# Kernel tuning notes

Measured on AMD Instinct MI355X. Metric: run time of the kernel, lower is better.

The kernel has to match this reference:

```python
import jax, jax.numpy as jnp
import numpy as np

N, E, D, L = 40000, 640000, 128, 4

def setup_inputs() -> dict:
    key = jax.random.key(0)
    ks = jax.random.split(key, 4)
    x = jax.random.normal(ks[0], (N, D), dtype=jnp.float32)
    edge_index = jax.random.randint(ks[1], (2, E), 0, N)
    edge_weight = jax.random.uniform(ks[2], (E,), dtype=jnp.float32)
    W = jax.random.normal(ks[3], (L, D, D), dtype=jnp.float32) / np.float32(np.sqrt(D))
    b = jnp.zeros((L, D), jnp.float32)
    gamma = jnp.ones((L, D), jnp.float32)
    beta = jnp.zeros((L, D), jnp.float32)
    return dict(x=x, edge_index=edge_index, edge_weight=edge_weight, W=W, b=b, gamma=gamma, beta=beta)

def _gcn_norm(edge_index, edge_weight, n):
    # PyG gcn_norm: add self loops (weight 1), symmetric D^-1/2 A D^-1/2
    loops = jnp.arange(n)
    src = jnp.concatenate([edge_index[0], loops])
    dst = jnp.concatenate([edge_index[1], loops])
    ew = jnp.concatenate([edge_weight, jnp.ones((n,), edge_weight.dtype)])
    deg = jax.ops.segment_sum(ew, dst, num_segments=n)
    dis = jnp.where(deg > 0, jax.lax.rsqrt(jnp.maximum(deg, 1e-12)), 0.0)
    return src, dst, dis[src] * ew * dis[dst]

def _batchnorm(h, g, bta):
    # training-mode BatchNorm1d over the node axis, biased variance, eps=1e-5
    mu = h.mean(0)
    var = h.var(0)
    return g * (h - mu) * jax.lax.rsqrt(var + 1e-5) + bta

def reference(x, edge_index, edge_weight, W, b, gamma, beta):
    n = x.shape[0]
    n_layers = W.shape[0]
    src, dst, norm = _gcn_norm(edge_index, edge_weight, n)
    x0 = x  # decoded_reshaped_x for skip connections
    for i in range(n_layers):
        h = x @ W[i]                                   # [N, D] linear (GCNConv.lin)
        msg = h[src] * norm[:, None]                   # gather + scale, [E+N, D]
        h = jax.ops.segment_sum(msg, dst, num_segments=n) + b[i]
        if i < n_layers - 1:
            h = jax.nn.relu(h)
        h = h + x0                                     # skip connection
        if i != n_layers - 2:
            h = _batchnorm(h, gamma[i], beta[i])
        x = h
    return x
```

## Files before the change

### kernel.cpp

```cpp
#include <hip/hip_runtime.h>
#include <cstdint>
#include <cstddef>

constexpr int N = 40000;
constexpr int E = 640000;
constexpr int D = 128;
constexpr int NBLK = (N + 255) / 256;
constexpr int NBKT = NBLK;
constexpr int BCAP = 5120;
constexpr int AGG_GRID = 2500;

typedef _Float16 half8 __attribute__((ext_vector_type(8)));
typedef float f32x4 __attribute__((ext_vector_type(4)));

__device__ __forceinline__ unsigned int pack_rec(int idx, float v) {
  union { _Float16 h; unsigned short us; } c; c.h = (_Float16)v;
  return (unsigned int)idx | ((unsigned int)c.us << 16);
}


__global__ void k_zero(uint4* __restrict__ p, uint4* __restrict__ q) {
  int i = blockIdx.x * 256 + threadIdx.x;
  if (i < 22096) p[i] = make_uint4(0u, 0u, 0u, 0u);
  else if (i < 22136) q[i - 22096] = make_uint4(0u, 0u, 0u, 0u);
}


__global__ void k_bigprep(const int* __restrict__ ei, const float* __restrict__ ew,
                          unsigned long long* __restrict__ packed,
                          const float* __restrict__ X, _Float16* __restrict__ Xh,
                          const float* __restrict__ W, _Float16* __restrict__ Wt,
                          unsigned long long* __restrict__ binned,
                          int* __restrict__ bktcnt) {
  int bid = blockIdx.x, t = threadIdx.x;
  if (bid < 313) {
    __shared__ int lhist[NBKT], lbase[NBKT], lrank[NBKT];
    if (t < NBKT) { lhist[t] = 0; lrank[t] = 0; }
    __syncthreads();
    int e8 = bid * 256 + t;
    bool act = (e8 < E / 8);
    int4 sa, sb, da, db; float4 wa, wb;
    if (act) {
      sa = ((const int4*)ei)[e8 * 2];
      sb = ((const int4*)ei)[e8 * 2 + 1];
      da = ((const int4*)(ei + E))[e8 * 2];
      db = ((const int4*)(ei + E))[e8 * 2 + 1];
      wa = ((const float4*)ew)[e8 * 2];
      wb = ((const float4*)ew)[e8 * 2 + 1];
      atomicAdd(&packed[da.x], (1ULL << 40) | (unsigned long long)__float2uint_rn(wa.x * 67108864.0f));
      atomicAdd(&packed[da.y], (1ULL << 40) | (unsigned long long)__float2uint_rn(wa.y * 67108864.0f));
      atomicAdd(&packed[da.z], (1ULL << 40) | (unsigned long long)__float2uint_rn(wa.z * 67108864.0f));
      atomicAdd(&packed[da.w], (1ULL << 40) | (unsigned long long)__float2uint_rn(wa.w * 67108864.0f));
      atomicAdd(&packed[db.x], (1ULL << 40) | (unsigned long long)__float2uint_rn(wb.x * 67108864.0f));
      atomicAdd(&packed[db.y], (1ULL << 40) | (unsigned long long)__float2uint_rn(wb.y * 67108864.0f));
      atomicAdd(&packed[db.z], (1ULL << 40) | (unsigned long long)__float2uint_rn(wb.z * 67108864.0f));
      atomicAdd(&packed[db.w], (1ULL << 40) | (unsigned long long)__float2uint_rn(wb.w * 67108864.0f));
      atomicAdd(&lhist[da.x >> 8], 1); atomicAdd(&lhist[da.y >> 8], 1);
      atomicAdd(&lhist[da.z >> 8], 1); atomicAdd(&lhist[da.w >> 8], 1);
      atomicAdd(&lhist[db.x >> 8], 1); atomicAdd(&lhist[db.y >> 8], 1);
      atomicAdd(&lhist[db.z >> 8], 1); atomicAdd(&lhist[db.w >> 8], 1);
    }
    __syncthreads();
    if (t < NBKT && lhist[t] > 0) lbase[t] = atomicAdd(&bktcnt[t], lhist[t]);
    __syncthreads();
    if (act) {
      auto emit = [&](int s, int dcol, float w) {
        int bkt = dcol >> 8;
        int rank = atomicAdd(&lrank[bkt], 1);
        int pos = lbase[bkt] + rank;
        unsigned long long rec = (unsigned long long)pack_rec(s, w)
                               | ((unsigned long long)(dcol & 255) << 32);
        if (pos < BCAP) binned[(size_t)bkt * BCAP + pos] = rec;
      };
      emit(sa.x, da.x, wa.x); emit(sa.y, da.y, wa.y);
      emit(sa.z, da.z, wa.z); emit(sa.w, da.w, wa.w);
      emit(sb.x, db.x, wb.x); emit(sb.y, db.y, wb.y);
      emit(sb.z, db.z, wb.z); emit(sb.w, db.w, wb.w);
    }
  } else if (bid < 2813) {
    int i = (bid - 313) * 256 + t;
    float4 v0 = ((const float4*)X)[i * 2];
    float4 v1 = ((const float4*)X)[i * 2 + 1];
    half8 h;
    h[0] = (_Float16)v0.x; h[1] = (_Float16)v0.y; h[2] = (_Float16)v0.z; h[3] = (_Float16)v0.w;
    h[4] = (_Float16)v1.x; h[5] = (_Float16)v1.y; h[6] = (_Float16)v1.z; h[7] = (_Float16)v1.w;
    ((half8*)Xh)[i] = h;
  } else {
    int o = (bid - 2813) * 256 + t;
    int l = o >> 14, rem = o & 16383, c = rem >> 7, k = rem & 127;
    Wt[o] = (_Float16)W[l * 16384 + k * 128 + c];
  }
}

__global__ __launch_bounds__(256) void k_partial(const unsigned long long* __restrict__ packed,
                                                 int* __restrict__ bsum) {
  __shared__ int red[256];
  int t = threadIdx.x;
  int i = blockIdx.x * 256 + t;
  red[t] = (i < N) ? ((int)(packed[i] >> 40) + 1) : 0;
  __syncthreads();
  for (int off = 128; off > 0; off >>= 1) {
    if (t < off) red[t] += red[t + off];
    __syncthreads();
  }
  if (t == 0) bsum[blockIdx.x] = red[0];
}

__global__ void k_scan_bsums(const int* __restrict__ bsum, int* __restrict__ bpre) {
  __shared__ int s[256];
  int t = threadIdx.x;
  s[t] = (t < NBLK) ? bsum[t] : 0;
  __syncthreads();
  for (int off = 1; off < 256; off <<= 1) {
    int v = s[t];
    int add = (t >= off) ? s[t - off] : 0;
    __syncthreads();
    s[t] = v + add;
    __syncthreads();
  }
  if (t < NBLK) bpre[t] = (t == 0) ? 0 : s[t - 1];
}

__global__ __launch_bounds__(256) void k_fill_offs(const unsigned long long* __restrict__ packed,
    const int* __restrict__ bpre, int* __restrict__ offs,
    unsigned int* __restrict__ cv, float* __restrict__ dis, int* __restrict__ hist) {
  __shared__ int s[256];
  __shared__ int lhist[64];
  int t = threadIdx.x;
  int i = blockIdx.x * 256 + t;
  if (t < 64) lhist[t] = 0;
  unsigned long long p = (i < N) ? packed[i] : 0ULL;
  int c = (i < N) ? ((int)(p >> 40) + 1) : 0;
  s[t] = c;
  __syncthreads();
  for (int off = 1; off < 256; off <<= 1) {
    int v = s[t];
    int add = (t >= off) ? s[t - off] : 0;
    __syncthreads();
    s[t] = v + add;
    __syncthreads();
  }
  if (i < N) {
    float deg = (float)(p & ((1ULL << 40) - 1)) * (1.0f / 67108864.0f);
    float ds = rsqrtf(deg + 1.0f);
    dis[i] = ds;
    int run = bpre[blockIdx.x] + s[t] - c;
    offs[i] = run;
    cv[run] = pack_rec(i, 1.0f);
    atomicAdd(&lhist[min(c, 63)], 1);
  }
  __syncthreads();
  if (t < 64 && lhist[t] > 0) atomicAdd(&hist[t], lhist[t]);
  if (i == N - 1) offs[N] = N + E;
}


__global__ void k_histscan(const int* __restrict__ hist, int* __restrict__ histstart,
                           int* __restrict__ histcur) {
  int b = threadIdx.x;
  int s = 0;
  for (int b2 = b + 1; b2 < 64; ++b2) s += hist[b2];
  histstart[b] = s;
  histcur[b] = s;
}


__device__ __forceinline__ void gemm_body(int bid, int tid, const _Float16* __restrict__ X,
    const _Float16* __restrict__ Wt, const float* __restrict__ sums,
    const float* __restrict__ gamma, const float* __restrict__ beta, int useBN,
    const float* __restrict__ dis, _Float16* __restrict__ Hout,
    float* scl, float* shf) {
  if (tid < 128) {
    if (useBN) {
      float s = 0.f, s2 = 0.f;
#pragma unroll
      for (int r = 0; r < 8; ++r) { s += sums[r * 256 + tid]; s2 += sums[r * 256 + 128 + tid]; }
      float mu = s * (1.0f / N);
      float var = s2 * (1.0f / N) - mu * mu;
      float rs = rsqrtf(var + 1e-5f);
      float sc = gamma[tid] * rs;
      scl[tid] = sc;
      shf[tid] = beta[tid] - mu * sc;
    } else {
      scl[tid] = 1.0f;
      shf[tid] = 0.0f;
    }
  }
  __syncthreads();

  int wv = tid >> 6, lane = tid & 63;
  int fr = lane & 15, kg = lane >> 4;
  int arow = bid * 64 + wv * 16 + fr;
  const _Float16* xrow = X + (size_t)arow * D;

  half8 af[4];
#pragma unroll
  for (int kc = 0; kc < 4; ++kc) {
    int k0 = kc * 32 + kg * 8;
    half8 xr = *(const half8*)&xrow[k0];
    half8 a;
#pragma unroll
    for (int u = 0; u < 8; ++u)
      a[u] = (_Float16)fmaf((float)xr[u], scl[k0 + u], shf[k0 + u]);
    af[kc] = a;
  }

  f32x4 acc[8];
#pragma unroll
  for (int ct = 0; ct < 8; ++ct) acc[ct] = (f32x4){0.f, 0.f, 0.f, 0.f};

#pragma unroll
  for (int ct = 0; ct < 8; ++ct) {
    const _Float16* wcol = Wt + (size_t)(ct * 16 + fr) * 128;
#pragma unroll
    for (int kc = 0; kc < 4; ++kc) {
      half8 bf = *(const half8*)&wcol[kc * 32 + kg * 8];
      acc[ct] = __builtin_amdgcn_mfma_f32_16x16x32_f16(af[kc], bf, acc[ct], 0, 0, 0);
    }
  }

  int orow0 = bid * 64 + wv * 16 + kg * 4;
#pragma unroll
  for (int rg = 0; rg < 4; ++rg) {
    int grow = orow0 + rg;
    float dsv = dis[grow];
    _Float16* hrow = Hout + (size_t)grow * D;
#pragma unroll
    for (int ct = 0; ct < 8; ++ct)
      hrow[ct * 16 + fr] = (_Float16)(acc[ct][rg] * dsv);
  }
}

__global__ __launch_bounds__(256) void k_gemm(const _Float16* __restrict__ X,
    const _Float16* __restrict__ Wt, const float* __restrict__ sums,
    const float* __restrict__ gamma, const float* __restrict__ beta, int useBN,
    const float* __restrict__ dis, _Float16* __restrict__ Hout) {
  __shared__ float scl[128], shf[128];
  gemm_body(blockIdx.x, threadIdx.x, X, Wt, sums, gamma, beta, useBN, dis, Hout, scl, shf);
}


__global__ __launch_bounds__(256) void k_gemm0_fill(const _Float16* __restrict__ X,
    const _Float16* __restrict__ Wt, const float* __restrict__ dis,
    _Float16* __restrict__ Hout,
    const int* __restrict__ offs, const unsigned long long* __restrict__ binned,
    const int* __restrict__ bktcnt, unsigned int* __restrict__ cv,
    const unsigned long long* __restrict__ packed, int* __restrict__ histcur,
    int* __restrict__ perm) {
  int bid = blockIdx.x, t = threadIdx.x;
  if (bid < 625) {
    __shared__ float scl[128], shf[128];
    gemm_body(bid, t, X, Wt, (const float*)nullptr, (const float*)nullptr,
              (const float*)nullptr, 0, dis, Hout, scl, shf);
  } else if (bid < 625 + NBKT) {
    int bkt = bid - 625;
    __shared__ int lcur[256];
    int row = bkt * 256 + t;
    lcur[t] = (row < N) ? (offs[row] + 1) : 0;
    __syncthreads();
    int cnt = min(bktcnt[bkt], BCAP);
    const unsigned long long* bp = binned + (size_t)bkt * BCAP;
    for (int e = t; e < cnt; e += 256) {
      unsigned long long r = bp[e];
      int local = (int)(r >> 32);
      int slot = atomicAdd(&lcur[local], 1);
      cv[slot] = (unsigned int)r;
    }
  } else {
    __shared__ int lhist[64], lbase[64];
    if (t < 64) lhist[t] = 0;
    __syncthreads();
    int i = (bid - (625 + NBKT)) * 256 + t;
    bool valid = (i < N);
    int bin = 0, myrank = 0;
    if (valid) {
      int c = (int)(packed[i] >> 40) + 1;
      bin = min(c, 63);
      myrank = atomicAdd(&lhist[bin], 1);
    }
    __syncthreads();
    if (t < 64 && lhist[t] > 0) lbase[t] = atomicAdd(&histcur[t], lhist[t]);
    __syncthreads();
    if (valid) perm[lbase[bin] + myrank] = i;
  }
}


__global__ __launch_bounds__(256) void k_agg(const uint4* __restrict__ Hu4,
    const int* __restrict__ offs, const unsigned int* __restrict__ cv,
    const float* __restrict__ dis, const float* __restrict__ bias,
    const uint4* __restrict__ x0h, const int* __restrict__ perm,
    int doRelu, int doStats, int outF32,
    _Float16* __restrict__ Hout16, float* __restrict__ Houtf, float* __restrict__ sums) {
  int t = threadIdx.x;
  int sl = t & 15;
  int g = t >> 4;
  int row = perm[blockIdx.x * 16 + g];
  float4 bv0 = ((const float4*)bias)[sl * 2];
  float4 bv1 = ((const float4*)bias)[sl * 2 + 1];

  int e0 = offs[row], e1 = offs[row + 1];
  float a[8];
#pragma unroll
  for (int k = 0; k < 8; ++k) a[k] = 0.f;
  for (int eb = e0; eb < e1; eb += 16) {
    int m = min(16, e1 - eb);
    unsigned int rec = 0;
    if (sl < m) rec = cv[eb + sl];
#pragma unroll 8
    for (int j = 0; j < m; ++j) {
      unsigned int rj = __shfl(rec, j, 16);
      int sj = (int)(rj & 0xFFFFu);
      union { unsigned short us; _Float16 h; } vh; vh.us = (unsigned short)(rj >> 16);
      float vj = (float)vh.h;
      union { uint4 u; _Float16 hh[8]; } cu;
      cu.u = Hu4[(size_t)sj * 16 + sl];
#pragma unroll
      for (int k = 0; k < 8; ++k) a[k] = fmaf((float)cu.hh[k], vj, a[k]);
    }
  }
  float dr = dis[row];
  union { uint4 u; _Float16 hh[8]; } xc;
  xc.u = x0h[(size_t)row * 16 + sl];
  float rr[8];
  rr[0] = fmaf(a[0], dr, bv0.x); rr[1] = fmaf(a[1], dr, bv0.y);
  rr[2] = fmaf(a[2], dr, bv0.z); rr[3] = fmaf(a[3], dr, bv0.w);
  rr[4] = fmaf(a[4], dr, bv1.x); rr[5] = fmaf(a[5], dr, bv1.y);
  rr[6] = fmaf(a[6], dr, bv1.z); rr[7] = fmaf(a[7], dr, bv1.w);
  if (doRelu) {
#pragma unroll
    for (int k = 0; k < 8; ++k) rr[k] = fmaxf(rr[k], 0.f);
  }
#pragma unroll
  for (int k = 0; k < 8; ++k) rr[k] += (float)xc.hh[k];
  if (outF32) {
    float4 o0, o1;
    o0.x = rr[0]; o0.y = rr[1]; o0.z = rr[2]; o0.w = rr[3];
    o1.x = rr[4]; o1.y = rr[5]; o1.z = rr[6]; o1.w = rr[7];
    ((float4*)Houtf)[(size_t)row * 32 + sl * 2] = o0;
    ((float4*)Houtf)[(size_t)row * 32 + sl * 2 + 1] = o1;
  } else {
    union { uint4 u; _Float16 hh[8]; } ov;
#pragma unroll
    for (int k = 0; k < 8; ++k) ov.hh[k] = (_Float16)rr[k];
    ((uint4*)Hout16)[(size_t)row * 16 + sl] = ov.u;
  }

  if (doStats) {
    __shared__ float reds[16 * 128], reds2[16 * 128];
#pragma unroll
    for (int k = 0; k < 8; ++k) {
      reds[g * 128 + sl * 8 + k] = rr[k];
      reds2[g * 128 + sl * 8 + k] = rr[k] * rr[k];
    }
    __syncthreads();
    if (t < 128) {
      float ts = 0.f, ts2 = 0.f;
#pragma unroll
      for (int j = 0; j < 16; ++j) { ts += reds[j * 128 + t]; ts2 += reds2[j * 128 + t]; }
      int rep = blockIdx.x & 7;
      atomicAdd(&sums[rep * 256 + t], ts);
      atomicAdd(&sums[rep * 256 + 128 + t], ts2);
    }
  }
}


__global__ __launch_bounds__(256) void k_bnapply(float* __restrict__ H,
    const float* __restrict__ sums, const float* __restrict__ gamma,
    const float* __restrict__ beta) {
  __shared__ float scl[128], shf[128];
  int t = threadIdx.x;
  if (t < 128) {
    float s = 0.f, s2 = 0.f;
#pragma unroll
    for (int r = 0; r < 8; ++r) { s += sums[r * 256 + t]; s2 += sums[r * 256 + 128 + t]; }
    float mu = s * (1.0f / N);
    float var = s2 * (1.0f / N) - mu * mu;
    float rs = rsqrtf(var + 1e-5f);
    float sc = gamma[t] * rs;
    scl[t] = sc;
    shf[t] = beta[t] - mu * sc;
  }
  __syncthreads();
  size_t i = (size_t)blockIdx.x * 256 + t;
  float4 v = ((const float4*)H)[i];
  int c = (int)(i & 31) * 4;
  v.x = fmaf(v.x, scl[c + 0], shf[c + 0]);
  v.y = fmaf(v.y, scl[c + 1], shf[c + 1]);
  v.z = fmaf(v.z, scl[c + 2], shf[c + 2]);
  v.w = fmaf(v.w, scl[c + 3], shf[c + 3]);
  ((float4*)H)[i] = v;
}


extern "C" void kernel_launch(void* const* d_in, const int* in_sizes, int n_in,
                              void* d_out, int out_size, void* d_ws, size_t ws_size,
                              hipStream_t stream) {
  const float* x     = (const float*)d_in[0];
  const int*   ei    = (const int*)d_in[1];
  const float* ew    = (const float*)d_in[2];
  const float* W     = (const float*)d_in[3];
  const float* b     = (const float*)d_in[4];
  const float* gamma = (const float*)d_in[5];
  const float* beta  = (const float*)d_in[6];
  float* out = (float*)d_out;

  char* ws = (char*)d_ws;
  _Float16* hlin   = (_Float16*)ws;
  _Float16* hagg16 = (_Float16*)(ws + 10240000);
  _Float16* xh     = (_Float16*)(ws + 20480000);
  unsigned long long* packed = (unsigned long long*)(ws + 30720000);
  float* sums4    = (float*)(ws + 31040000);
  int*   hist     = (int*)  (ws + 31072768);
  int*   histstart= (int*)  (ws + 31073024);
  int*   histcur  = (int*)  (ws + 31073280);
  float* dis      = (float*)(ws + 31073536);
  int*   offs     = (int*)  (ws + 31233536);
  int*   bktcnt   = (int*)  (ws + 31393552);
  unsigned int* cv= (unsigned int*)(ws + 31553552);
  int*   perm     = (int*)  (ws + 34273552);
  int*   bsum     = (int*)  (ws + 34433552);
  int*   bpre     = (int*)  (ws + 34434192);
  _Float16* Wt    = (_Float16*)(ws + 34434832);
  unsigned long long* binned = (unsigned long long*)(ws + 34565904);

  k_zero<<<87, 256, 0, stream>>>((uint4*)packed, (uint4*)bktcnt);
  k_bigprep<<<3069, 256, 0, stream>>>(ei, ew, packed, x, xh, W, Wt, binned, bktcnt);
  k_partial<<<NBLK, 256, 0, stream>>>(packed, bsum);
  k_scan_bsums<<<1, 256, 0, stream>>>(bsum, bpre);
  k_fill_offs<<<NBLK, 256, 0, stream>>>(packed, bpre, offs, cv, dis, hist);
  k_histscan<<<1, 64, 0, stream>>>(hist, histstart, histcur);

  for (int l = 0; l < 4; ++l) {
    const _Float16* xin = (l == 0) ? xh : hagg16;
    if (l == 0) {
      k_gemm0_fill<<<625 + NBKT + 157, 256, 0, stream>>>(xin, Wt, dis, hlin,
                                                         offs, binned, bktcnt, cv,
                                                         packed, histcur, perm);
    } else {
      int useBN = (l == 1 || l == 2) ? 1 : 0;
      const float* sprev = sums4 + (size_t)(l - 1) * 2048;
      k_gemm<<<N / 64, 256, 0, stream>>>(xin, Wt + (size_t)l * 16384, sprev,
                                         gamma + (size_t)(l - 1) * D,
                                         beta + (size_t)(l - 1) * D, useBN, dis, hlin);
    }
    int doStats = (l != 2) ? 1 : 0;
    int doRelu = (l < 3) ? 1 : 0;
    int outF32 = (l == 3) ? 1 : 0;
    k_agg<<<AGG_GRID, 256, 0, stream>>>((const uint4*)hlin, offs, cv, dis,
                                        b + (size_t)l * D, (const uint4*)xh, perm,
                                        doRelu, doStats, outF32, hagg16, out,
                                        sums4 + (size_t)l * 2048);
  }
  k_bnapply<<<(N * D / 4) / 256, 256, 0, stream>>>(out, sums4 + 3 * 2048,
                                                   gamma + 3 * D, beta + 3 * D);
}
```

Before: 262.7 us.

## Compute node degrees per bucket in shared memory instead of global atomics

Result: faster. 232.7 us (-11.4%).

```diff
diff --git a/kernel.cpp b/kernel.cpp
--- a/kernel.cpp
+++ b/kernel.cpp
@@ -5,13 +5,13 @@
 constexpr int N = 40000;
 constexpr int E = 640000;
 constexpr int D = 128;
-constexpr int NBLK = (N + 255) / 256;
-constexpr int NBKT = NBLK;
+constexpr int NBKT = 157;
 constexpr int BCAP = 5120;
 constexpr int AGG_GRID = 2500;
 
 typedef _Float16 half8 __attribute__((ext_vector_type(8)));
 typedef float f32x4 __attribute__((ext_vector_type(4)));
+typedef unsigned long long ull;
 
 __device__ __forceinline__ unsigned int pack_rec(int idx, float v) {
   union { _Float16 h; unsigned short us; } c; c.h = (_Float16)v;
@@ -19,46 +19,36 @@
 }
 
 
-__global__ void k_zero(uint4* __restrict__ p, uint4* __restrict__ q) {
+__global__ void k_zero(uint4* __restrict__ p) {
   int i = blockIdx.x * 256 + threadIdx.x;
-  if (i < 22096) p[i] = make_uint4(0u, 0u, 0u, 0u);
-  else if (i < 22136) q[i - 22096] = make_uint4(0u, 0u, 0u, 0u);
+  if (i < 2136) p[i] = make_uint4(0u, 0u, 0u, 0u);
 }
 
 
 __global__ void k_bigprep(const int* __restrict__ ei, const float* __restrict__ ew,
-                          unsigned long long* __restrict__ packed,
                           const float* __restrict__ X, _Float16* __restrict__ Xh,
                           const float* __restrict__ W, _Float16* __restrict__ Wt,
-                          unsigned long long* __restrict__ binned,
-                          int* __restrict__ bktcnt) {
+                          ull* __restrict__ binned, int* __restrict__ bktcnt) {
   int bid = blockIdx.x, t = threadIdx.x;
-  if (bid < 313) {
+  if (bid < NBKT) {
     __shared__ int lhist[NBKT], lbase[NBKT], lrank[NBKT];
     if (t < NBKT) { lhist[t] = 0; lrank[t] = 0; }
     __syncthreads();
-    int e8 = bid * 256 + t;
-    bool act = (e8 < E / 8);
-    int4 sa, sb, da, db; float4 wa, wb;
+    int e16 = bid * 256 + t;
+    bool act = (e16 < E / 16);
+    int4 s4[4], d4[4]; float4 w4[4];
     if (act) {
-      sa = ((const int4*)ei)[e8 * 2];
-      sb = ((const int4*)ei)[e8 * 2 + 1];
-      da = ((const int4*)(ei + E))[e8 * 2];
-      db = ((const int4*)(ei + E))[e8 * 2 + 1];
-      wa = ((const float4*)ew)[e8 * 2];
-      wb = ((const float4*)ew)[e8 * 2 + 1];
-      atomicAdd(&packed[da.x], (1ULL << 40) | (unsigned long long)__float2uint_rn(wa.x * 67108864.0f));
-      atomicAdd(&packed[da.y], (1ULL << 40) | (unsigned long long)__float2uint_rn(wa.y * 67108864.0f));
-      atomicAdd(&packed[da.z], (1ULL << 40) | (unsigned long long)__float2uint_rn(wa.z * 67108864.0f));
-      atomicAdd(&packed[da.w], (1ULL << 40) | (unsigned long long)__float2uint_rn(wa.w * 67108864.0f));
-      atomicAdd(&packed[db.x], (1ULL << 40) | (unsigned long long)__float2uint_rn(wb.x * 67108864.0f));
-      atomicAdd(&packed[db.y], (1ULL << 40) | (unsigned long long)__float2uint_rn(wb.y * 67108864.0f));
-      atomicAdd(&packed[db.z], (1ULL << 40) | (unsigned long long)__float2uint_rn(wb.z * 67108864.0f));
-      atomicAdd(&packed[db.w], (1ULL << 40) | (unsigned long long)__float2uint_rn(wb.w * 67108864.0f));
-      atomicAdd(&lhist[da.x >> 8], 1); atomicAdd(&lhist[da.y >> 8], 1);
-      atomicAdd(&lhist[da.z >> 8], 1); atomicAdd(&lhist[da.w >> 8], 1);
-      atomicAdd(&lhist[db.x >> 8], 1); atomicAdd(&lhist[db.y >> 8], 1);
-      atomicAdd(&lhist[db.z >> 8], 1); atomicAdd(&lhist[db.w >> 8], 1);
+#pragma unroll
+      for (int u = 0; u < 4; ++u) {
+        s4[u] = ((const int4*)ei)[e16 * 4 + u];
+        d4[u] = ((const int4*)(ei + E))[e16 * 4 + u];
+        w4[u] = ((const float4*)ew)[e16 * 4 + u];
+      }
+#pragma unroll
+      for (int u = 0; u < 4; ++u) {
+        atomicAdd(&lhist[d4[u].x >> 8], 1); atomicAdd(&lhist[d4[u].y >> 8], 1);
+        atomicAdd(&lhist[d4[u].z >> 8], 1); atomicAdd(&lhist[d4[u].w >> 8], 1);
+      }
     }
     __syncthreads();
     if (t < NBKT && lhist[t] > 0) lbase[t] = atomicAdd(&bktcnt[t], lhist[t]);
@@ -68,17 +58,19 @@
         int bkt = dcol >> 8;
         int rank = atomicAdd(&lrank[bkt], 1);
         int pos = lbase[bkt] + rank;
-        unsigned long long rec = (unsigned long long)pack_rec(s, w)
-                               | ((unsigned long long)(dcol & 255) << 32);
+        ull rec = (ull)(unsigned)(s & 0xFFFF)
+                | ((ull)(unsigned)(dcol & 255) << 16)
+                | ((ull)__float2uint_rn(w * 67108864.0f) << 24);
         if (pos < BCAP) binned[(size_t)bkt * BCAP + pos] = rec;
       };
-      emit(sa.x, da.x, wa.x); emit(sa.y, da.y, wa.y);
-      emit(sa.z, da.z, wa.z); emit(sa.w, da.w, wa.w);
-      emit(sb.x, db.x, wb.x); emit(sb.y, db.y, wb.y);
-      emit(sb.z, db.z, wb.z); emit(sb.w, db.w, wb.w);
-    }
-  } else if (bid < 2813) {
-    int i = (bid - 313) * 256 + t;
+#pragma unroll
+      for (int u = 0; u < 4; ++u) {
+        emit(s4[u].x, d4[u].x, w4[u].x); emit(s4[u].y, d4[u].y, w4[u].y);
+        emit(s4[u].z, d4[u].z, w4[u].z); emit(s4[u].w, d4[u].w, w4[u].w);
+      }
+    }
+  } else if (bid < 2657) {
+    int i = (bid - NBKT) * 256 + t;
     float4 v0 = ((const float4*)X)[i * 2];
     float4 v1 = ((const float4*)X)[i * 2 + 1];
     half8 h;
@@ -86,30 +78,55 @@
     h[4] = (_Float16)v1.x; h[5] = (_Float16)v1.y; h[6] = (_Float16)v1.z; h[7] = (_Float16)v1.w;
     ((half8*)Xh)[i] = h;
   } else {
-    int o = (bid - 2813) * 256 + t;
+    int o = (bid - 2657) * 256 + t;
     int l = o >> 14, rem = o & 16383, c = rem >> 7, k = rem & 127;
     Wt[o] = (_Float16)W[l * 16384 + k * 128 + c];
   }
 }
 
-__global__ __launch_bounds__(256) void k_partial(const unsigned long long* __restrict__ packed,
-                                                 int* __restrict__ bsum) {
+
+__global__ __launch_bounds__(256) void k_bstats(const ull* __restrict__ binned,
+    const int* __restrict__ bktcnt, float* __restrict__ dis, int* __restrict__ rowc,
+    int* __restrict__ bsum, int* __restrict__ hist) {
+  __shared__ ull acc[256];
+  __shared__ int lhist[64];
   __shared__ int red[256];
-  int t = threadIdx.x;
-  int i = blockIdx.x * 256 + t;
-  red[t] = (i < N) ? ((int)(packed[i] >> 40) + 1) : 0;
+  int bkt = blockIdx.x, t = threadIdx.x;
+  acc[t] = 0ULL;
+  if (t < 64) lhist[t] = 0;
+  __syncthreads();
+  int cnt = min(bktcnt[bkt], BCAP);
+  const ull* bp = binned + (size_t)bkt * BCAP;
+  for (int e = t; e < cnt; e += 256) {
+    ull r = bp[e];
+    int local = (int)((r >> 16) & 255);
+    atomicAdd(&acc[local], (1ULL << 40) | (r >> 24));
+  }
+  __syncthreads();
+  int row = bkt * 256 + t;
+  int c = 0;
+  if (row < N) {
+    ull a = acc[t];
+    c = (int)(a >> 40) + 1;
+    float deg = (float)(a & ((1ULL << 40) - 1)) * (1.0f / 67108864.0f);
+    dis[row] = rsqrtf(deg + 1.0f);
+    rowc[row] = c;
+    atomicAdd(&lhist[min(c, 63)], 1);
+  }
+  red[t] = c;
   __syncthreads();
   for (int off = 128; off > 0; off >>= 1) {
     if (t < off) red[t] += red[t + off];
     __syncthreads();
   }
-  if (t == 0) bsum[blockIdx.x] = red[0];
+  if (t == 0) bsum[bkt] = red[0];
+  if (t < 64 && lhist[t] > 0) atomicAdd(&hist[t], lhist[t]);
 }
 
 __global__ void k_scan_bsums(const int* __restrict__ bsum, int* __restrict__ bpre) {
   __shared__ int s[256];
   int t = threadIdx.x;
-  s[t] = (t < NBLK) ? bsum[t] : 0;
+  s[t] = (t < NBKT) ? bsum[t] : 0;
   __syncthreads();
   for (int off = 1; off < 256; off <<= 1) {
     int v = s[t];
@@ -118,40 +135,7 @@
     s[t] = v + add;
     __syncthreads();
   }
-  if (t < NBLK) bpre[t] = (t == 0) ? 0 : s[t - 1];
-}
-
-__global__ __launch_bounds__(256) void k_fill_offs(const unsigned long long* __restrict__ packed,
-    const int* __restrict__ bpre, int* __restrict__ offs,
-    unsigned int* __restrict__ cv, float* __restrict__ dis, int* __restrict__ hist) {
-  __shared__ int s[256];
-  __shared__ int lhist[64];
-  int t = threadIdx.x;
-  int i = blockIdx.x * 256 + t;
-  if (t < 64) lhist[t] = 0;
-  unsigned long long p = (i < N) ? packed[i] : 0ULL;
-  int c = (i < N) ? ((int)(p >> 40) + 1) : 0;
-  s[t] = c;
-  __syncthreads();
-  for (int off = 1; off < 256; off <<= 1) {
-    int v = s[t];
-    int add = (t >= off) ? s[t - off] : 0;
-    __syncthreads();
-    s[t] = v + add;
-    __syncthreads();
-  }
-  if (i < N) {
-    float deg = (float)(p & ((1ULL << 40) - 1)) * (1.0f / 67108864.0f);
-    float ds = rsqrtf(deg + 1.0f);
-    dis[i] = ds;
-    int run = bpre[blockIdx.x] + s[t] - c;
-    offs[i] = run;
-    cv[run] = pack_rec(i, 1.0f);
-    atomicAdd(&lhist[min(c, 63)], 1);
-  }
-  __syncthreads();
-  if (t < 64 && lhist[t] > 0) atomicAdd(&hist[t], lhist[t]);
-  if (i == N - 1) offs[N] = N + E;
+  if (t < NBKT) bpre[t] = (t == 0) ? 0 : s[t - 1];
 }
 
 
@@ -243,10 +227,10 @@
 __global__ __launch_bounds__(256) void k_gemm0_fill(const _Float16* __restrict__ X,
     const _Float16* __restrict__ Wt, const float* __restrict__ dis,
     _Float16* __restrict__ Hout,
-    const int* __restrict__ offs, const unsigned long long* __restrict__ binned,
-    const int* __restrict__ bktcnt, unsigned int* __restrict__ cv,
-    const unsigned long long* __restrict__ packed, int* __restrict__ histcur,
-    int* __restrict__ perm) {
+    const int* __restrict__ rowc, const int* __restrict__ bpre,
+    const ull* __restrict__ binned, const int* __restrict__ bktcnt,
+    unsigned int* __restrict__ cv, int* __restrict__ offs,
+    int* __restrict__ histcur, int* __restrict__ perm) {
   int bid = blockIdx.x, t = threadIdx.x;
   if (bid < 625) {
     __shared__ float scl[128], shf[128];
@@ -255,16 +239,37 @@
   } else if (bid < 625 + NBKT) {
     int bkt = bid - 625;
     __shared__ int lcur[256];
+    __shared__ int s[256];
     int row = bkt * 256 + t;
-    lcur[t] = (row < N) ? (offs[row] + 1) : 0;
+    int c = (row < N) ? rowc[row] : 0;
+    s[t] = c;
+    __syncthreads();
+    for (int off = 1; off < 256; off <<= 1) {
+      int v = s[t];
+      int add = (t >= off) ? s[t - off] : 0;
+      __syncthreads();
+      s[t] = v + add;
+      __syncthreads();
+    }
+    int run = bpre[bkt] + s[t] - c;
+    if (row < N) {
+      offs[row] = run;
+      cv[run] = pack_rec(row, 1.0f);
+      lcur[t] = run + 1;
+    } else {
+      lcur[t] = 0;
+    }
+    if (row == N - 1) offs[N] = N + E;
     __syncthreads();
     int cnt = min(bktcnt[bkt], BCAP);
-    const unsigned long long* bp = binned + (size_t)bkt * BCAP;
+    const ull* bp = binned + (size_t)bkt * BCAP;
     for (int e = t; e < cnt; e += 256) {
-      unsigned long long r = bp[e];
-      int local = (int)(r >> 32);
+      ull r = bp[e];
+      int local = (int)((r >> 16) & 255);
+      int srcv = (int)(r & 0xFFFFu);
+      float w = (float)(unsigned)(r >> 24) * (1.0f / 67108864.0f);
       int slot = atomicAdd(&lcur[local], 1);
-      cv[slot] = (unsigned int)r;
+      cv[slot] = pack_rec(srcv, w);
     }
   } else {
     __shared__ int lhist[64], lbase[64];
@@ -274,7 +279,7 @@
     bool valid = (i < N);
     int bin = 0, myrank = 0;
     if (valid) {
-      int c = (int)(packed[i] >> 40) + 1;
+      int c = rowc[i];
       bin = min(c, 63);
       myrank = atomicAdd(&lhist[bin], 1);
     }
@@ -410,34 +415,33 @@
   _Float16* hlin   = (_Float16*)ws;
   _Float16* hagg16 = (_Float16*)(ws + 10240000);
   _Float16* xh     = (_Float16*)(ws + 20480000);
-  unsigned long long* packed = (unsigned long long*)(ws + 30720000);
-  float* sums4    = (float*)(ws + 31040000);
-  int*   hist     = (int*)  (ws + 31072768);
-  int*   histstart= (int*)  (ws + 31073024);
-  int*   histcur  = (int*)  (ws + 31073280);
-  float* dis      = (float*)(ws + 31073536);
-  int*   offs     = (int*)  (ws + 31233536);
-  int*   bktcnt   = (int*)  (ws + 31393552);
-  unsigned int* cv= (unsigned int*)(ws + 31553552);
-  int*   perm     = (int*)  (ws + 34273552);
-  int*   bsum     = (int*)  (ws + 34433552);
-  int*   bpre     = (int*)  (ws + 34434192);
-  _Float16* Wt    = (_Float16*)(ws + 34434832);
-  unsigned long long* binned = (unsigned long long*)(ws + 34565904);
-
-  k_zero<<<87, 256, 0, stream>>>((uint4*)packed, (uint4*)bktcnt);
-  k_bigprep<<<3069, 256, 0, stream>>>(ei, ew, packed, x, xh, W, Wt, binned, bktcnt);
-  k_partial<<<NBLK, 256, 0, stream>>>(packed, bsum);
+  float* sums4    = (float*)(ws + 30720000);
+  int*   hist     = (int*)  (ws + 30752768);
+  int*   histstart= (int*)  (ws + 30753024);
+  int*   histcur  = (int*)  (ws + 30753280);
+  int*   bktcnt   = (int*)  (ws + 30753536);
+  float* dis      = (float*)(ws + 30754176);
+  int*   offs     = (int*)  (ws + 30914176);
+  int*   rowc     = (int*)  (ws + 31074192);
+  unsigned int* cv= (unsigned int*)(ws + 31234192);
+  int*   perm     = (int*)  (ws + 33954192);
+  int*   bsum     = (int*)  (ws + 34114192);
+  int*   bpre     = (int*)  (ws + 34114832);
+  _Float16* Wt    = (_Float16*)(ws + 34115472);
+  ull* binned     = (ull*)  (ws + 34246544);
+
+  k_zero<<<9, 256, 0, stream>>>((uint4*)sums4);
+  k_bigprep<<<2913, 256, 0, stream>>>(ei, ew, x, xh, W, Wt, binned, bktcnt);
+  k_bstats<<<NBKT, 256, 0, stream>>>(binned, bktcnt, dis, rowc, bsum, hist);
   k_scan_bsums<<<1, 256, 0, stream>>>(bsum, bpre);
-  k_fill_offs<<<NBLK, 256, 0, stream>>>(packed, bpre, offs, cv, dis, hist);
   k_histscan<<<1, 64, 0, stream>>>(hist, histstart, histcur);
 
   for (int l = 0; l < 4; ++l) {
     const _Float16* xin = (l == 0) ? xh : hagg16;
     if (l == 0) {
       k_gemm0_fill<<<625 + NBKT + 157, 256, 0, stream>>>(xin, Wt, dis, hlin,
-                                                         offs, binned, bktcnt, cv,
-                                                         packed, histcur, perm);
+                                                         rowc, bpre, binned, bktcnt,
+                                                         cv, offs, histcur, perm);
     } else {
       int useBN = (l == 1 || l == 2) ? 1 : 0;
       const float* sprev = sums4 + (size_t)(l - 1) * 2048;
```
